# Performance work log

Hardware: AMD Instinct MI355X
Metric: run time of the kernel (lower is better)

## Reference

```python
import jax, jax.numpy as jnp
import numpy as np

B, T, S, D_MODEL = 2, 16, 512, 768
N_HEADS, HEAD_DIM = 12, 64
N_LATENTS = 32


def build_encoder_mask(modality_ids, n_latents):
    # encoder mode: latent queries attend everything; non-latent queries attend same-modality only
    S = modality_ids.shape[0]
    is_q_lat = (jnp.arange(S) < n_latents)[:, None]            # (S,1)
    same_mod = modality_ids[:, None] == modality_ids[None, :]  # (S,S)
    return jnp.where(is_q_lat, True, same_mod)                 # (S,S) bool


def setup_inputs() -> dict:
    key = jax.random.key(0)
    ks = jax.random.split(key, 9)
    x = jax.random.normal(ks[0], (B, T, S, D_MODEL), jnp.float32)
    w_scale = 1.0 / np.sqrt(D_MODEL)
    # flax MultiHeadDotProductAttention param layout: qkv kernels (D, H, head_dim), out kernel (H, head_dim, D)
    Wq = jax.random.normal(ks[1], (D_MODEL, N_HEADS, HEAD_DIM), jnp.float32) * w_scale
    Wk = jax.random.normal(ks[2], (D_MODEL, N_HEADS, HEAD_DIM), jnp.float32) * w_scale
    Wv = jax.random.normal(ks[3], (D_MODEL, N_HEADS, HEAD_DIM), jnp.float32) * w_scale
    Wo = jax.random.normal(ks[4], (N_HEADS, HEAD_DIM, D_MODEL), jnp.float32) * w_scale
    bq = jnp.zeros((N_HEADS, HEAD_DIM), jnp.float32)
    bk = jnp.zeros((N_HEADS, HEAD_DIM), jnp.float32)
    bv = jnp.zeros((N_HEADS, HEAD_DIM), jnp.float32)
    bo = jnp.zeros((D_MODEL,), jnp.float32)
    # 32 latent tokens (id -1), then 240 tokens of modality 0 and 240 of modality 1
    modality_ids = jnp.concatenate([
        jnp.full((N_LATENTS,), -1, jnp.int32),
        jnp.zeros((240,), jnp.int32),
        jnp.ones((240,), jnp.int32),
    ])
    return dict(x=x, Wq=Wq, bq=bq, Wk=Wk, bk=bk, Wv=Wv, bv=bv, Wo=Wo, bo=bo,
                modality_ids=modality_ids, n_latents=N_LATENTS)


def reference(x, Wq, bq, Wk, bk, Wv, bv, Wo, bo, modality_ids, n_latents):
    B, T, S, D = x.shape
    H, hd = Wq.shape[1], Wq.shape[2]
    xf = x.reshape(B * T, S, D)                                   # (BT,S,D)
    q = (jnp.einsum('bsd,dhk->bshk', xf, Wq) + bq) / jnp.sqrt(jnp.asarray(hd, x.dtype))
    k = jnp.einsum('bsd,dhk->bshk', xf, Wk) + bk
    v = jnp.einsum('bsd,dhk->bshk', xf, Wv) + bv
    scores = jnp.einsum('bqhd,bkhd->bhqk', q, k)                  # (BT,H,S,S)
    mask = build_encoder_mask(modality_ids, n_latents)            # (S,S)
    neg = jnp.finfo(x.dtype).min
    scores = jnp.where(mask[None, None], scores, neg)
    attn = jax.nn.softmax(scores, axis=-1)
    ctx = jnp.einsum('bhqk,bkhd->bqhd', attn, v)                  # (BT,S,H,hd)
    y = jnp.einsum('bqhd,hdo->bqo', ctx, Wo) + bo                 # (BT,S,D)
    return y.reshape(B, T, S, D)
```

## Files before the change

### kernel.cpp

```cpp
#include <hip/hip_runtime.h>
#include <hip/hip_bf16.h>
#include <stdint.h>

#define BT_N  32
#define SEQL  512
#define DM    768
#define NHEAD 12
#define HDIM  64
#define MTOT  (BT_N * SEQL)

typedef __bf16 bf16x8 __attribute__((ext_vector_type(8)));
typedef float  f32x4  __attribute__((ext_vector_type(4)));

__device__ __forceinline__ float b2f(uint16_t u)  { return __uint_as_float(((uint32_t)u) << 16); }
__device__ __forceinline__ uint16_t f2b(float f) {
    uint32_t u = __float_as_uint(f);
    return (uint16_t)((u + 0x7fffu + ((u >> 16) & 1u)) >> 16);
}
__device__ __forceinline__ void split_bf16(float x, uint16_t& hi, uint16_t& lo) {
    hi = f2b(x);
    lo = f2b(x - b2f(hi));
}

__global__ __launch_bounds__(256) void split_x_kernel(
    const float* __restrict__ X, uint16_t* __restrict__ Xh, uint16_t* __restrict__ Xl)
{
    size_t i = ((size_t)blockIdx.x * 256 + threadIdx.x) * 4;
    float4 v = *(const float4*)(X + i);
    float xx[4] = {v.x, v.y, v.z, v.w};
    ushort4 h, l;
    uint16_t hh, ll;
    split_bf16(xx[0], hh, ll); h.x = hh; l.x = ll;
    split_bf16(xx[1], hh, ll); h.y = hh; l.y = ll;
    split_bf16(xx[2], hh, ll); h.z = hh; l.z = ll;
    split_bf16(xx[3], hh, ll); h.w = hh; l.w = ll;
    *(ushort4*)(Xh + i) = h;
    *(ushort4*)(Xl + i) = l;
}

__global__ __launch_bounds__(256) void wprep_kernel(
    const float* __restrict__ Wq, const float* __restrict__ Wk,
    const float* __restrict__ Wv, const float* __restrict__ Wo,
    uint16_t* __restrict__ WqTh, uint16_t* __restrict__ WqTl,
    uint16_t* __restrict__ WkTh, uint16_t* __restrict__ WkTl,
    uint16_t* __restrict__ WvT,  uint16_t* __restrict__ WoT)
{
    __shared__ float tile[32][33];
    const int z = blockIdx.z;
    const float* W; uint16_t* Th; uint16_t* Tl;
    if (z == 0)      { W = Wq; Th = WqTh; Tl = WqTl; }
    else if (z == 1) { W = Wk; Th = WkTh; Tl = WkTl; }
    else if (z == 2) { W = Wv; Th = WvT;  Tl = nullptr; }
    else             { W = Wo; Th = WoT;  Tl = nullptr; }

    const int k0 = blockIdx.x * 32, n0 = blockIdx.y * 32;
    const int tid = threadIdx.x;
    {
        int r = tid >> 3, c = (tid & 7) * 4;
        *(float4*)&tile[r][c] = *(const float4*)(W + (size_t)(k0 + r) * DM + n0 + c);
    }
    __syncthreads();
    {
        int nl = tid >> 3, kk = (tid & 7) * 4;
        ushort4 h, l;
        uint16_t hh, ll;
        float v0 = tile[kk + 0][nl], v1 = tile[kk + 1][nl];
        float v2 = tile[kk + 2][nl], v3 = tile[kk + 3][nl];
        split_bf16(v0, hh, ll); h.x = hh; l.x = ll;
        split_bf16(v1, hh, ll); h.y = hh; l.y = ll;
        split_bf16(v2, hh, ll); h.z = hh; l.z = ll;
        split_bf16(v3, hh, ll); h.w = hh; l.w = ll;
        size_t o = (size_t)(n0 + nl) * DM + k0 + kk;
        *(ushort4*)(Th + o) = h;
        if (Tl) *(ushort4*)(Tl + o) = l;
    }
}

__global__ __launch_bounds__(256) void qkv_gemm_v3(
    const uint16_t* __restrict__ Xh, const uint16_t* __restrict__ Xl,
    const uint16_t* __restrict__ WqTh, const uint16_t* __restrict__ WqTl,
    const uint16_t* __restrict__ WkTh, const uint16_t* __restrict__ WkTl,
    const uint16_t* __restrict__ WvT,
    const float* __restrict__ bq, const float* __restrict__ bk, const float* __restrict__ bv,
    uint16_t* __restrict__ Qh, uint16_t* __restrict__ Ql,
    uint16_t* __restrict__ Kh, uint16_t* __restrict__ Kl,
    uint16_t* __restrict__ Vt)
{
    __shared__ uint16_t AhS[128][72], AlS[128][72];
    __shared__ uint16_t BhS[64][72],  BlS[64][72];

    const int m0 = blockIdx.x * 128;
    const int n0 = blockIdx.y * 64;
    const int z  = blockIdx.z;

    const uint16_t* Bh_g; const uint16_t* Bl_g = nullptr; const float* bias;
    if (z == 0)      { Bh_g = WqTh; Bl_g = WqTl; bias = bq; }
    else if (z == 1) { Bh_g = WkTh; Bl_g = WkTl; bias = bk; }
    else             { Bh_g = WvT;               bias = bv; }

    const int tid  = threadIdx.x;
    const int lane = tid & 63, wave = tid >> 6;
    const int quad = lane >> 4, l16 = lane & 15;
    const int wq = wave * 32;

    f32x4 acc[2][4];
    #pragma unroll
    for (int t = 0; t < 2; t++)
        #pragma unroll
        for (int nt = 0; nt < 4; nt++) acc[t][nt] = (f32x4){0.f,0.f,0.f,0.f};

    const int sr = tid >> 3, sc = (tid & 7) * 8;

    for (int k0 = 0; k0 < DM; k0 += 64) {
        __syncthreads();
        #pragma unroll
        for (int i = 0; i < 4; i++) {
            int r = i * 32 + sr;
            *(uint4*)&AhS[r][sc] = *(const uint4*)(Xh + (size_t)(m0 + r) * DM + k0 + sc);
        }
        #pragma unroll
        for (int i = 0; i < 2; i++) {
            int r = i * 32 + sr;
            *(uint4*)&BhS[r][sc] = *(const uint4*)(Bh_g + (size_t)(n0 + r) * DM + k0 + sc);
        }
        if (z < 2) {
            #pragma unroll
            for (int i = 0; i < 4; i++) {
                int r = i * 32 + sr;
                *(uint4*)&AlS[r][sc] = *(const uint4*)(Xl + (size_t)(m0 + r) * DM + k0 + sc);
            }
            #pragma unroll
            for (int i = 0; i < 2; i++) {
                int r = i * 32 + sr;
                *(uint4*)&BlS[r][sc] = *(const uint4*)(Bl_g + (size_t)(n0 + r) * DM + k0 + sc);
            }
        }
        __syncthreads();
        #pragma unroll
        for (int ksub = 0; ksub < 2; ksub++) {
            bf16x8 ah[2], bh[4];
            ah[0] = *(const bf16x8*)&AhS[wq + l16][ksub * 32 + quad * 8];
            ah[1] = *(const bf16x8*)&AhS[wq + 16 + l16][ksub * 32 + quad * 8];
            #pragma unroll
            for (int nt = 0; nt < 4; nt++)
                bh[nt] = *(const bf16x8*)&BhS[nt * 16 + l16][ksub * 32 + quad * 8];
            if (z < 2) {
                bf16x8 al[2], bl[4];
                al[0] = *(const bf16x8*)&AlS[wq + l16][ksub * 32 + quad * 8];
                al[1] = *(const bf16x8*)&AlS[wq + 16 + l16][ksub * 32 + quad * 8];
                #pragma unroll
                for (int nt = 0; nt < 4; nt++)
                    bl[nt] = *(const bf16x8*)&BlS[nt * 16 + l16][ksub * 32 + quad * 8];
                #pragma unroll
                for (int t = 0; t < 2; t++)
                    #pragma unroll
                    for (int nt = 0; nt < 4; nt++) {
                        acc[t][nt] = __builtin_amdgcn_mfma_f32_16x16x32_bf16(al[t], bh[nt], acc[t][nt], 0, 0, 0);
                        acc[t][nt] = __builtin_amdgcn_mfma_f32_16x16x32_bf16(ah[t], bl[nt], acc[t][nt], 0, 0, 0);
                        acc[t][nt] = __builtin_amdgcn_mfma_f32_16x16x32_bf16(ah[t], bh[nt], acc[t][nt], 0, 0, 0);
                    }
            } else {
                #pragma unroll
                for (int t = 0; t < 2; t++)
                    #pragma unroll
                    for (int nt = 0; nt < 4; nt++)
                        acc[t][nt] = __builtin_amdgcn_mfma_f32_16x16x32_bf16(ah[t], bh[nt], acc[t][nt], 0, 0, 0);
            }
        }
    }

    const float scale = (z == 0) ? 0.125f : 1.0f;
    uint16_t* OutH = (z == 0) ? Qh : Kh;
    uint16_t* OutL = (z == 0) ? Ql : Kl;
    #pragma unroll
    for (int t = 0; t < 2; t++) {
        #pragma unroll
        for (int nt = 0; nt < 4; nt++) {
            int n = n0 + nt * 16 + l16;
            float bsv = bias[n];
            int hh = n >> 6, d = n & 63;
            int mbase = m0 + wq + t * 16 + quad * 4;
            if (z == 2) {
                int bt = mbase >> 9, sb = mbase & 511;
                ushort4 pk;
                pk.x = f2b(acc[t][nt][0] + bsv);
                pk.y = f2b(acc[t][nt][1] + bsv);
                pk.z = f2b(acc[t][nt][2] + bsv);
                pk.w = f2b(acc[t][nt][3] + bsv);
                *(ushort4*)&Vt[(((size_t)bt * NHEAD + hh) * HDIM + d) * SEQL + sb] = pk;
            } else {
                #pragma unroll
                for (int r = 0; r < 4; r++) {
                    int m = mbase + r;
                    float val = (acc[t][nt][r] + bsv) * scale;
                    uint16_t vh, vl; split_bf16(val, vh, vl);
                    int bt = m >> 9, s = m & 511;
                    size_t idx = (((size_t)bt * NHEAD + hh) * SEQL + s) * HDIM + d;
                    OutH[idx] = vh; OutL[idx] = vl;
                }
            }
        }
    }
}

__global__ __launch_bounds__(256) void out_proj_v2(
    const uint16_t* __restrict__ A, const uint16_t* __restrict__ WoT,
    const float* __restrict__ bias, float* __restrict__ Y)
{
    __shared__ uint16_t As[128][72];
    __shared__ uint16_t Bs[64][72];

    const int m0 = blockIdx.x * 128;
    const int n0 = blockIdx.y * 64;
    const int tid  = threadIdx.x;
    const int lane = tid & 63, wave = tid >> 6;
    const int quad = lane >> 4, l16 = lane & 15;
    const int wq = wave * 32;

    f32x4 acc[2][4];
    #pragma unroll
    for (int t = 0; t < 2; t++)
        #pragma unroll
        for (int nt = 0; nt < 4; nt++) acc[t][nt] = (f32x4){0.f,0.f,0.f,0.f};

    const int sr = tid >> 3, sc = (tid & 7) * 8;

    for (int k0 = 0; k0 < DM; k0 += 64) {
        __syncthreads();
        #pragma unroll
        for (int i = 0; i < 4; i++) {
            int r = i * 32 + sr;
            *(uint4*)&As[r][sc] = *(const uint4*)(A + (size_t)(m0 + r) * DM + k0 + sc);
        }
        #pragma unroll
        for (int i = 0; i < 2; i++) {
            int r = i * 32 + sr;
            *(uint4*)&Bs[r][sc] = *(const uint4*)(WoT + (size_t)(n0 + r) * DM + k0 + sc);
        }
        __syncthreads();
        #pragma unroll
        for (int ksub = 0; ksub < 2; ksub++) {
            bf16x8 a0 = *(const bf16x8*)&As[wq + l16][ksub * 32 + quad * 8];
            bf16x8 a1 = *(const bf16x8*)&As[wq + 16 + l16][ksub * 32 + quad * 8];
            bf16x8 bf[4];
            #pragma unroll
            for (int nt = 0; nt < 4; nt++)
                bf[nt] = *(const bf16x8*)&Bs[nt * 16 + l16][ksub * 32 + quad * 8];
            #pragma unroll
            for (int nt = 0; nt < 4; nt++) {
                acc[0][nt] = __builtin_amdgcn_mfma_f32_16x16x32_bf16(a0, bf[nt], acc[0][nt], 0, 0, 0);
                acc[1][nt] = __builtin_amdgcn_mfma_f32_16x16x32_bf16(a1, bf[nt], acc[1][nt], 0, 0, 0);
            }
        }
    }

    #pragma unroll
    for (int t = 0; t < 2; t++) {
        #pragma unroll
        for (int nt = 0; nt < 4; nt++) {
            int n = n0 + nt * 16 + l16;
            float bsv = bias[n];
            #pragma unroll
            for (int r = 0; r < 4; r++) {
                int m = m0 + wq + t * 16 + quad * 4 + r;
                Y[(size_t)m * DM + n] = acc[t][nt][r] + bsv;
            }
        }
    }
}

#define QTILE 128

__global__ __launch_bounds__(256) void attn_mfma_kernel(
    const uint16_t* __restrict__ Qhg, const uint16_t* __restrict__ Qlg,
    const uint16_t* __restrict__ Khg, const uint16_t* __restrict__ Klg,
    const uint16_t* __restrict__ Vtg, const int* __restrict__ modality,
    const int* __restrict__ nlat_p, uint16_t* __restrict__ ctx)
{
    __shared__ uint16_t KhS[64][72];
    __shared__ uint16_t KlS[64][72];
    __shared__ uint16_t Vs[64][72];
    __shared__ uint16_t Ps[QTILE][72];
    __shared__ int modk_s[64];

    const int bh = blockIdx.x;
    const int bt = bh / NHEAD, h = bh % NHEAD;
    const int q0 = blockIdx.y * QTILE;
    const int tid = threadIdx.x, lane = tid & 63, wave = tid >> 6;
    const int quad = lane >> 4, l16 = lane & 15;
    const int wq = wave * 32;

    const size_t hb = (size_t)bh * SEQL * HDIM;
    const int nlat = nlat_p[0];

    bf16x8 qh[2][2], ql[2][2];
    #pragma unroll
    for (int t = 0; t < 2; t++)
        #pragma unroll
        for (int ks = 0; ks < 2; ks++) {
            size_t o = hb + (size_t)(q0 + wq + t*16 + l16) * HDIM + ks*32 + quad*8;
            qh[t][ks] = *(const bf16x8*)(Qhg + o);
            ql[t][ks] = *(const bf16x8*)(Qlg + o);
        }

    int  mq[2][4]; bool lat_[2][4];
    #pragma unroll
    for (int t = 0; t < 2; t++)
        #pragma unroll
        for (int r = 0; r < 4; r++) {
            int row = q0 + wq + t*16 + quad*4 + r;
            mq[t][r]   = modality[row];
            lat_[t][r] = row < nlat;
        }

    float mrow[2][4], lrow[2][4];
    #pragma unroll
    for (int t = 0; t < 2; t++)
        #pragma unroll
        for (int r = 0; r < 4; r++) { mrow[t][r] = -3e38f; lrow[t][r] = 0.f; }
    f32x4 O[2][4];
    #pragma unroll
    for (int t = 0; t < 2; t++)
        #pragma unroll
        for (int dt = 0; dt < 4; dt++) O[t][dt] = (f32x4){0.f,0.f,0.f,0.f};

    for (int s0 = 0; s0 < SEQL; s0 += 64) {
        __syncthreads();
        {
            int rr = tid >> 2, c0 = (tid & 3) * 16;
            const uint16_t* kp = Khg + hb + (size_t)(s0 + rr) * HDIM + c0;
            const uint16_t* lp = Klg + hb + (size_t)(s0 + rr) * HDIM + c0;
            const uint16_t* vp = Vtg + hb + (size_t)rr * SEQL + s0 + c0;
            *(uint4*)&KhS[rr][c0]     = *(const uint4*)kp;
            *(uint4*)&KhS[rr][c0 + 8] = *((const uint4*)kp + 1);
            *(uint4*)&KlS[rr][c0]     = *(const uint4*)lp;
            *(uint4*)&KlS[rr][c0 + 8] = *((const uint4*)lp + 1);
            *(uint4*)&Vs[rr][c0]      = *(const uint4*)vp;
            *(uint4*)&Vs[rr][c0 + 8]  = *((const uint4*)vp + 1);
        }
        if (tid < 64) modk_s[tid] = modality[s0 + tid];
        __syncthreads();

        f32x4 S[2][4];
        #pragma unroll
        for (int t = 0; t < 2; t++)
            #pragma unroll
            for (int n = 0; n < 4; n++) S[t][n] = (f32x4){0.f,0.f,0.f,0.f};
        #pragma unroll
        for (int n = 0; n < 4; n++) {
            #pragma unroll
            for (int ks = 0; ks < 2; ks++) {
                bf16x8 kh = *(const bf16x8*)&KhS[n*16 + l16][ks*32 + quad*8];
                bf16x8 kl = *(const bf16x8*)&KlS[n*16 + l16][ks*32 + quad*8];
                #pragma unroll
                for (int t = 0; t < 2; t++) {
                    S[t][n] = __builtin_amdgcn_mfma_f32_16x16x32_bf16(ql[t][ks], kh, S[t][n], 0, 0, 0);
                    S[t][n] = __builtin_amdgcn_mfma_f32_16x16x32_bf16(qh[t][ks], kl, S[t][n], 0, 0, 0);
                    S[t][n] = __builtin_amdgcn_mfma_f32_16x16x32_bf16(qh[t][ks], kh, S[t][n], 0, 0, 0);
                }
            }
        }

        int mk[4];
        #pragma unroll
        for (int n = 0; n < 4; n++) mk[n] = modk_s[n*16 + l16];
        #pragma unroll
        for (int t = 0; t < 2; t++)
            #pragma unroll
            for (int n = 0; n < 4; n++)
                #pragma unroll
                for (int r = 0; r < 4; r++)
                    if (!(lat_[t][r] || (mq[t][r] == mk[n]))) S[t][n][r] = -3e38f;

        #pragma unroll
        for (int t = 0; t < 2; t++) {
            #pragma unroll
            for (int r = 0; r < 4; r++) {
                float mc = fmaxf(fmaxf(S[t][0][r], S[t][1][r]),
                                 fmaxf(S[t][2][r], S[t][3][r]));
                #pragma unroll
                for (int off = 1; off <= 8; off <<= 1)
                    mc = fmaxf(mc, __shfl_xor(mc, off, 64));
                float mo = mrow[t][r];
                float mn = fmaxf(mo, mc);
                float al = __expf(mo - mn);
                float g  = (mn <= -1e37f) ? 0.f : 1.f;
                float sum = 0.f;
                #pragma unroll
                for (int n = 0; n < 4; n++) {
                    float p = __expf(S[t][n][r] - mn) * g;
                    Ps[wq + t*16 + quad*4 + r][n*16 + l16] = f2b(p);
                    sum += p;
                }
                #pragma unroll
                for (int off = 1; off <= 8; off <<= 1)
                    sum += __shfl_xor(sum, off, 64);
                lrow[t][r] = lrow[t][r] * al + sum;
                mrow[t][r] = mn;
                #pragma unroll
                for (int dt = 0; dt < 4; dt++) O[t][dt][r] *= al;
            }
        }

        #pragma unroll
        for (int ks = 0; ks < 2; ks++) {
            bf16x8 pa[2];
            #pragma unroll
            for (int t = 0; t < 2; t++)
                pa[t] = *(const bf16x8*)&Ps[wq + t*16 + l16][ks*32 + quad*8];
            #pragma unroll
            for (int dt = 0; dt < 4; dt++) {
                bf16x8 vb = *(const bf16x8*)&Vs[dt*16 + l16][ks*32 + quad*8];
                #pragma unroll
                for (int t = 0; t < 2; t++)
                    O[t][dt] = __builtin_amdgcn_mfma_f32_16x16x32_bf16(pa[t], vb, O[t][dt], 0, 0, 0);
            }
        }
    }

    #pragma unroll
    for (int t = 0; t < 2; t++) {
        float inv[4];
        #pragma unroll
        for (int r = 0; r < 4; r++) inv[r] = 1.0f / fmaxf(lrow[t][r], 1e-30f);
        #pragma unroll
        for (int dt = 0; dt < 4; dt++) {
            #pragma unroll
            for (int r = 0; r < 4; r++) {
                int row = q0 + wq + t*16 + quad*4 + r;
                ctx[(size_t)(bt * SEQL + row) * DM + h*HDIM + dt*16 + l16] =
                    f2b(O[t][dt][r] * inv[r]);
            }
        }
    }
}

extern "C" void kernel_launch(void* const* d_in, const int* in_sizes, int n_in,
                              void* d_out, int out_size, void* d_ws, size_t ws_size,
                              hipStream_t stream) {
    const float* X  = (const float*)d_in[0];
    const float* Wq = (const float*)d_in[1];
    const float* bq = (const float*)d_in[2];
    const float* Wk = (const float*)d_in[3];
    const float* bk = (const float*)d_in[4];
    const float* Wv = (const float*)d_in[5];
    const float* bv = (const float*)d_in[6];
    const float* Wo = (const float*)d_in[7];
    const float* bo = (const float*)d_in[8];
    const int* modality = (const int*)d_in[9];
    const int* nlat     = (const int*)d_in[10];

    const size_t per = (size_t)MTOT * DM;
    const size_t wsz = (size_t)DM * DM;
    uint16_t* p = (uint16_t*)d_ws;
    uint16_t* Xh   = p; p += per;
    uint16_t* Xl   = p; p += per;
    uint16_t* WqTh = p; p += wsz;
    uint16_t* WqTl = p; p += wsz;
    uint16_t* WkTh = p; p += wsz;
    uint16_t* WkTl = p; p += wsz;
    uint16_t* WvT  = p; p += wsz;
    uint16_t* WoT  = p; p += wsz;
    uint16_t* Qh   = p; p += per;
    uint16_t* Ql   = p; p += per;
    uint16_t* Kh   = p; p += per;
    uint16_t* Kl   = p; p += per;
    uint16_t* Vt   = p; p += per;
    uint16_t* c_ws = Xh;

    split_x_kernel<<<dim3(per / 1024), 256, 0, stream>>>(X, Xh, Xl);
    wprep_kernel<<<dim3(DM / 32, DM / 32, 4), 256, 0, stream>>>(
        Wq, Wk, Wv, Wo, WqTh, WqTl, WkTh, WkTl, WvT, WoT);
    qkv_gemm_v3<<<dim3(MTOT / 128, DM / 64, 3), 256, 0, stream>>>(
        Xh, Xl, WqTh, WqTl, WkTh, WkTl, WvT, bq, bk, bv, Qh, Ql, Kh, Kl, Vt);
    attn_mfma_kernel<<<dim3(BT_N * NHEAD, SEQL / QTILE), 256, 0, stream>>>(
        Qh, Ql, Kh, Kl, Vt, modality, nlat, c_ws);
    out_proj_v2<<<dim3(MTOT / 128, DM / 64), 256, 0, stream>>>(
        c_ws, WoT, bo, (float*)d_out);
}
```

Measured before the change: 475.3 us.

## Rewrite projection GEMMs with 128x128 tiles, double-buffered direct-to-LDS loads and swizzle

The QKV and output projection GEMMs are rebuilt around 128x128 block tiles with a 2x2 wave layout. Global tiles are loaded straight into LDS with global_load_lds into two ping-pong buffers, so the next tile's loads overlap the current tile's MFMAs. An XOR swizzle on the LDS layout avoids bank conflicts. The V projection, which needs only the hi part, moves into its own kernel so the split-precision Q/K path carries no per-iteration branch. The larger tiles raise register pressure, and the launch bound of 2 blocks per SM plus the fixed iteration counts tie the kernels to these exact dimensions.

```diff
diff --git a/kernel.cpp b/kernel.cpp
--- a/kernel.cpp
+++ b/kernel.cpp
@@ -1,5 +1,4 @@
 #include <hip/hip_runtime.h>
-#include <hip/hip_bf16.h>
 #include <stdint.h>
 
 #define BT_N  32
@@ -20,6 +19,13 @@
 __device__ __forceinline__ void split_bf16(float x, uint16_t& hi, uint16_t& lo) {
     hi = f2b(x);
     lo = f2b(x - b2f(hi));
+}
+
+__device__ __forceinline__ void gload16(const void* g, void* l) {
+    __builtin_amdgcn_global_load_lds(
+        (const __attribute__((address_space(1))) void*)g,
+        (__attribute__((address_space(3))) void*)l,
+        16, 0, 0);
 }
 
 __global__ __launch_bounds__(256) void split_x_kernel(
@@ -76,195 +82,318 @@
     }
 }
 
-__global__ __launch_bounds__(256) void qkv_gemm_v3(
+__global__ __launch_bounds__(256, 2) void qk_gemm_split(
     const uint16_t* __restrict__ Xh, const uint16_t* __restrict__ Xl,
     const uint16_t* __restrict__ WqTh, const uint16_t* __restrict__ WqTl,
     const uint16_t* __restrict__ WkTh, const uint16_t* __restrict__ WkTl,
-    const uint16_t* __restrict__ WvT,
-    const float* __restrict__ bq, const float* __restrict__ bk, const float* __restrict__ bv,
+    const float* __restrict__ bq, const float* __restrict__ bk,
     uint16_t* __restrict__ Qh, uint16_t* __restrict__ Ql,
-    uint16_t* __restrict__ Kh, uint16_t* __restrict__ Kl,
-    uint16_t* __restrict__ Vt)
+    uint16_t* __restrict__ Kh, uint16_t* __restrict__ Kl)
 {
-    __shared__ uint16_t AhS[128][72], AlS[128][72];
-    __shared__ uint16_t BhS[64][72],  BlS[64][72];
+    __shared__ uint16_t lds[2][16384];
 
     const int m0 = blockIdx.x * 128;
-    const int n0 = blockIdx.y * 64;
+    const int n0 = blockIdx.y * 128;
     const int z  = blockIdx.z;
 
-    const uint16_t* Bh_g; const uint16_t* Bl_g = nullptr; const float* bias;
-    if (z == 0)      { Bh_g = WqTh; Bl_g = WqTl; bias = bq; }
-    else if (z == 1) { Bh_g = WkTh; Bl_g = WkTl; bias = bk; }
-    else             { Bh_g = WvT;               bias = bv; }
+    const uint16_t* Bh_g = z ? WkTh : WqTh;
+    const uint16_t* Bl_g = z ? WkTl : WqTl;
+    const float* bias    = z ? bk : bq;
+    uint16_t* OutH       = z ? Kh : Qh;
+    uint16_t* OutL       = z ? Kl : Ql;
+    const float scale    = z ? 1.0f : 0.125f;
 
     const int tid  = threadIdx.x;
     const int lane = tid & 63, wave = tid >> 6;
     const int quad = lane >> 4, l16 = lane & 15;
-    const int wq = wave * 32;
-
-    f32x4 acc[2][4];
-    #pragma unroll
-    for (int t = 0; t < 2; t++)
-        #pragma unroll
-        for (int nt = 0; nt < 4; nt++) acc[t][nt] = (f32x4){0.f,0.f,0.f,0.f};
-
-    const int sr = tid >> 3, sc = (tid & 7) * 8;
-
-    for (int k0 = 0; k0 < DM; k0 += 64) {
+    const int wm = (wave >> 1) * 64, wn = (wave & 1) * 64;
+
+    const uint16_t* src[8];
+    #pragma unroll
+    for (int i = 0; i < 8; i++) {
+        int d    = (i * 256 + tid) * 16;
+        int row  = (d >> 7) & 127;
+        int colb = d & 127;
+        int scol = colb ^ ((row & 7) << 4);
+        int kofs = (scol & 63) >> 1;
+        const uint16_t* g;
+        if (d < 16384) g = (scol < 64 ? Xh : Xl)     + (size_t)(m0 + row) * DM + kofs;
+        else           g = (scol < 64 ? Bh_g : Bl_g) + (size_t)(n0 + row) * DM + kofs;
+        src[i] = g;
+    }
+
+    int offA[4], offB[4];
+    #pragma unroll
+    for (int i = 0; i < 4; i++) {
+        int r  = wm + i * 16 + l16;
+        offA[i] = r * 64 + (((quad * 16) ^ ((r & 7) << 4)) >> 1);
+        int rb = wn + i * 16 + l16;
+        offB[i] = 8192 + rb * 64 + (((quad * 16) ^ ((rb & 7) << 4)) >> 1);
+    }
+
+    f32x4 acc[4][4];
+    #pragma unroll
+    for (int i = 0; i < 4; i++)
+        #pragma unroll
+        for (int j = 0; j < 4; j++) acc[i][j] = (f32x4){0.f,0.f,0.f,0.f};
+
+    auto stage = [&](int buf) {
+        #pragma unroll
+        for (int i = 0; i < 8; i++) {
+            gload16(src[i], &lds[buf][(i * 256 + wave * 64) * 8]);
+            src[i] += 32;
+        }
+    };
+    auto computeTile = [&](int buf) {
+        const uint16_t* base = &lds[buf][0];
+        bf16x8 ah[4], al[4], bh[4], bl[4];
+        #pragma unroll
+        for (int i = 0; i < 4; i++) {
+            ah[i] = *(const bf16x8*)(base + offA[i]);
+            al[i] = *(const bf16x8*)(base + (offA[i] ^ 32));
+            bh[i] = *(const bf16x8*)(base + offB[i]);
+            bl[i] = *(const bf16x8*)(base + (offB[i] ^ 32));
+        }
+        #pragma unroll
+        for (int mi = 0; mi < 4; mi++)
+            #pragma unroll
+            for (int ni = 0; ni < 4; ni++) {
+                acc[mi][ni] = __builtin_amdgcn_mfma_f32_16x16x32_bf16(al[mi], bh[ni], acc[mi][ni], 0, 0, 0);
+                acc[mi][ni] = __builtin_amdgcn_mfma_f32_16x16x32_bf16(ah[mi], bl[ni], acc[mi][ni], 0, 0, 0);
+                acc[mi][ni] = __builtin_amdgcn_mfma_f32_16x16x32_bf16(ah[mi], bh[ni], acc[mi][ni], 0, 0, 0);
+            }
+    };
+
+    stage(0);
+    asm volatile("s_waitcnt vmcnt(0)" ::: "memory");
+    __syncthreads();
+
+    int cur = 0;
+    for (int t = 0; t < 23; t++) {
+        stage(cur ^ 1);
+        computeTile(cur);
+        asm volatile("s_waitcnt vmcnt(0)" ::: "memory");
         __syncthreads();
+        cur ^= 1;
+    }
+    computeTile(cur);
+
+    #pragma unroll
+    for (int i = 0; i < 4; i++) {
+        #pragma unroll
+        for (int j = 0; j < 4; j++) {
+            int n = n0 + wn + j * 16 + l16;
+            float bsv = bias[n];
+            int hh = n >> 6, dd = n & 63;
+            int mb = m0 + wm + i * 16 + quad * 4;
+            #pragma unroll
+            for (int r = 0; r < 4; r++) {
+                int m = mb + r;
+                float val = (acc[i][j][r] + bsv) * scale;
+                uint16_t vh, vl; split_bf16(val, vh, vl);
+                int bt = m >> 9, s = m & 511;
+                size_t idx = (((size_t)bt * NHEAD + hh) * SEQL + s) * HDIM + dd;
+                OutH[idx] = vh; OutL[idx] = vl;
+            }
+        }
+    }
+}
+
+__global__ __launch_bounds__(256, 2) void v_gemm_plain(
+    const uint16_t* __restrict__ Xh, const uint16_t* __restrict__ WvT,
+    const float* __restrict__ bv, uint16_t* __restrict__ Vt)
+{
+    __shared__ uint16_t lds[2][16384];
+
+    const int m0 = blockIdx.x * 128;
+    const int n0 = blockIdx.y * 128;
+    const int tid  = threadIdx.x;
+    const int lane = tid & 63, wave = tid >> 6;
+    const int quad = lane >> 4, l16 = lane & 15;
+    const int wm = (wave >> 1) * 64, wn = (wave & 1) * 64;
+
+    const uint16_t* src[8];
+    #pragma unroll
+    for (int i = 0; i < 8; i++) {
+        int d    = (i * 256 + tid) * 16;
+        int row  = (d >> 7) & 127;
+        int colb = d & 127;
+        int scol = colb ^ ((row & 7) << 4);
+        int kofs = scol >> 1;
+        src[i] = (d < 16384 ? Xh + (size_t)(m0 + row) * DM
+                            : WvT + (size_t)(n0 + row) * DM) + kofs;
+    }
+
+    int offA[4], offB[4];
+    #pragma unroll
+    for (int i = 0; i < 4; i++) {
+        int r  = wm + i * 16 + l16;
+        offA[i] = r * 64 + (((quad * 16) ^ ((r & 7) << 4)) >> 1);
+        int rb = wn + i * 16 + l16;
+        offB[i] = 8192 + rb * 64 + (((quad * 16) ^ ((rb & 7) << 4)) >> 1);
+    }
+
+    f32x4 acc[4][4];
+    #pragma unroll
+    for (int i = 0; i < 4; i++)
+        #pragma unroll
+        for (int j = 0; j < 4; j++) acc[i][j] = (f32x4){0.f,0.f,0.f,0.f};
+
+    auto stage = [&](int buf) {
+        #pragma unroll
+        for (int i = 0; i < 8; i++) {
+            gload16(src[i], &lds[buf][(i * 256 + wave * 64) * 8]);
+            src[i] += 64;
+        }
+    };
+    auto computeTile = [&](int buf) {
+        const uint16_t* base = &lds[buf][0];
+        bf16x8 a0[4], a1[4], b0[4], b1[4];
         #pragma unroll
         for (int i = 0; i < 4; i++) {
-            int r = i * 32 + sr;
-            *(uint4*)&AhS[r][sc] = *(const uint4*)(Xh + (size_t)(m0 + r) * DM + k0 + sc);
-        }
-        #pragma unroll
-        for (int i = 0; i < 2; i++) {
-            int r = i * 32 + sr;
-            *(uint4*)&BhS[r][sc] = *(const uint4*)(Bh_g + (size_t)(n0 + r) * DM + k0 + sc);
-        }
-        if (z < 2) {
-            #pragma unroll
-            for (int i = 0; i < 4; i++) {
-                int r = i * 32 + sr;
-                *(uint4*)&AlS[r][sc] = *(const uint4*)(Xl + (size_t)(m0 + r) * DM + k0 + sc);
-            }
-            #pragma unroll
-            for (int i = 0; i < 2; i++) {
-                int r = i * 32 + sr;
-                *(uint4*)&BlS[r][sc] = *(const uint4*)(Bl_g + (size_t)(n0 + r) * DM + k0 + sc);
-            }
-        }
+            a0[i] = *(const bf16x8*)(base + offA[i]);
+            a1[i] = *(const bf16x8*)(base + (offA[i] ^ 32));
+            b0[i] = *(const bf16x8*)(base + offB[i]);
+            b1[i] = *(const bf16x8*)(base + (offB[i] ^ 32));
+        }
+        #pragma unroll
+        for (int mi = 0; mi < 4; mi++)
+            #pragma unroll
+            for (int ni = 0; ni < 4; ni++)
+                acc[mi][ni] = __builtin_amdgcn_mfma_f32_16x16x32_bf16(a0[mi], b0[ni], acc[mi][ni], 0, 0, 0);
+        #pragma unroll
+        for (int mi = 0; mi < 4; mi++)
+            #pragma unroll
+            for (int ni = 0; ni < 4; ni++)
+                acc[mi][ni] = __builtin_amdgcn_mfma_f32_16x16x32_bf16(a1[mi], b1[ni], acc[mi][ni], 0, 0, 0);
+    };
+
+    stage(0);
+    asm volatile("s_waitcnt vmcnt(0)" ::: "memory");
+    __syncthreads();
+
+    int cur = 0;
+    for (int t = 0; t < 11; t++) {
+        stage(cur ^ 1);
+        computeTile(cur);
+        asm volatile("s_waitcnt vmcnt(0)" ::: "memory");
         __syncthreads();
-        #pragma unroll
-        for (int ksub = 0; ksub < 2; ksub++) {
-            bf16x8 ah[2], bh[4];
-            ah[0] = *(const bf16x8*)&AhS[wq + l16][ksub * 32 + quad * 8];
-            ah[1] = *(const bf16x8*)&AhS[wq + 16 + l16][ksub * 32 + quad * 8];
-            #pragma unroll
-            for (int nt = 0; nt < 4; nt++)
-                bh[nt] = *(const bf16x8*)&BhS[nt * 16 + l16][ksub * 32 + quad * 8];
-            if (z < 2) {
-                bf16x8 al[2], bl[4];
-                al[0] = *(const bf16x8*)&AlS[wq + l16][ksub * 32 + quad * 8];
-                al[1] = *(const bf16x8*)&AlS[wq + 16 + l16][ksub * 32 + quad * 8];
-                #pragma unroll
-                for (int nt = 0; nt < 4; nt++)
-                    bl[nt] = *(const bf16x8*)&BlS[nt * 16 + l16][ksub * 32 + quad * 8];
-                #pragma unroll
-                for (int t = 0; t < 2; t++)
-                    #pragma unroll
-                    for (int nt = 0; nt < 4; nt++) {
-                        acc[t][nt] = __builtin_amdgcn_mfma_f32_16x16x32_bf16(al[t], bh[nt], acc[t][nt], 0, 0, 0);
-                        acc[t][nt] = __builtin_amdgcn_mfma_f32_16x16x32_bf16(ah[t], bl[nt], acc[t][nt], 0, 0, 0);
-                        acc[t][nt] = __builtin_amdgcn_mfma_f32_16x16x32_bf16(ah[t], bh[nt], acc[t][nt], 0, 0, 0);
-                    }
-            } else {
-                #pragma unroll
-                for (int t = 0; t < 2; t++)
-                    #pragma unroll
-                    for (int nt = 0; nt < 4; nt++)
-                        acc[t][nt] = __builtin_amdgcn_mfma_f32_16x16x32_bf16(ah[t], bh[nt], acc[t][nt], 0, 0, 0);
-            }
-        }
-    }
-
-    const float scale = (z == 0) ? 0.125f : 1.0f;
-    uint16_t* OutH = (z == 0) ? Qh : Kh;
-    uint16_t* OutL = (z == 0) ? Ql : Kl;
-    #pragma unroll
-    for (int t = 0; t < 2; t++) {
-        #pragma unroll
-        for (int nt = 0; nt < 4; nt++) {
-            int n = n0 + nt * 16 + l16;
-            float bsv = bias[n];
-            int hh = n >> 6, d = n & 63;
-            int mbase = m0 + wq + t * 16 + quad * 4;
-            if (z == 2) {
-                int bt = mbase >> 9, sb = mbase & 511;
-                ushort4 pk;
-                pk.x = f2b(acc[t][nt][0] + bsv);
-                pk.y = f2b(acc[t][nt][1] + bsv);
-                pk.z = f2b(acc[t][nt][2] + bsv);
-                pk.w = f2b(acc[t][nt][3] + bsv);
-                *(ushort4*)&Vt[(((size_t)bt * NHEAD + hh) * HDIM + d) * SEQL + sb] = pk;
-            } else {
-                #pragma unroll
-                for (int r = 0; r < 4; r++) {
-                    int m = mbase + r;
-                    float val = (acc[t][nt][r] + bsv) * scale;
-                    uint16_t vh, vl; split_bf16(val, vh, vl);
-                    int bt = m >> 9, s = m & 511;
-                    size_t idx = (((size_t)bt * NHEAD + hh) * SEQL + s) * HDIM + d;
-                    OutH[idx] = vh; OutL[idx] = vl;
-                }
-            }
-        }
-    }
-}
-
-__global__ __launch_bounds__(256) void out_proj_v2(
+        cur ^= 1;
+    }
+    computeTile(cur);
+
+    #pragma unroll
+    for (int i = 0; i < 4; i++) {
+        #pragma unroll
+        for (int j = 0; j < 4; j++) {
+            int n = n0 + wn + j * 16 + l16;
+            float bsv = bv[n];
+            int hh = n >> 6, dd = n & 63;
+            int mb = m0 + wm + i * 16 + quad * 4;
+            int bt = mb >> 9, sb = mb & 511;
+            ushort4 pk;
+            pk.x = f2b(acc[i][j][0] + bsv);
+            pk.y = f2b(acc[i][j][1] + bsv);
+            pk.z = f2b(acc[i][j][2] + bsv);
+            pk.w = f2b(acc[i][j][3] + bsv);
+            *(ushort4*)&Vt[(((size_t)bt * NHEAD + hh) * HDIM + dd) * SEQL + sb] = pk;
+        }
+    }
+}
+
+__global__ __launch_bounds__(256, 2) void out_proj_v3(
     const uint16_t* __restrict__ A, const uint16_t* __restrict__ WoT,
     const float* __restrict__ bias, float* __restrict__ Y)
 {
-    __shared__ uint16_t As[128][72];
-    __shared__ uint16_t Bs[64][72];
+    __shared__ uint16_t lds[2][16384];
 
     const int m0 = blockIdx.x * 128;
-    const int n0 = blockIdx.y * 64;
+    const int n0 = blockIdx.y * 128;
     const int tid  = threadIdx.x;
     const int lane = tid & 63, wave = tid >> 6;
     const int quad = lane >> 4, l16 = lane & 15;
-    const int wq = wave * 32;
-
-    f32x4 acc[2][4];
-    #pragma unroll
-    for (int t = 0; t < 2; t++)
-        #pragma unroll
-        for (int nt = 0; nt < 4; nt++) acc[t][nt] = (f32x4){0.f,0.f,0.f,0.f};
-
-    const int sr = tid >> 3, sc = (tid & 7) * 8;
-
-    for (int k0 = 0; k0 < DM; k0 += 64) {
+    const int wm = (wave >> 1) * 64, wn = (wave & 1) * 64;
+
+    const uint16_t* src[8];
+    #pragma unroll
+    for (int i = 0; i < 8; i++) {
+        int d    = (i * 256 + tid) * 16;
+        int row  = (d >> 7) & 127;
+        int colb = d & 127;
+        int scol = colb ^ ((row & 7) << 4);
+        int kofs = scol >> 1;
+        src[i] = (d < 16384 ? A + (size_t)(m0 + row) * DM
+                            : WoT + (size_t)(n0 + row) * DM) + kofs;
+    }
+
+    int offA[4], offB[4];
+    #pragma unroll
+    for (int i = 0; i < 4; i++) {
+        int r  = wm + i * 16 + l16;
+        offA[i] = r * 64 + (((quad * 16) ^ ((r & 7) << 4)) >> 1);
+        int rb = wn + i * 16 + l16;
+        offB[i] = 8192 + rb * 64 + (((quad * 16) ^ ((rb & 7) << 4)) >> 1);
+    }
+
+    f32x4 acc[4][4];
+    #pragma unroll
+    for (int i = 0; i < 4; i++)
+        #pragma unroll
+        for (int j = 0; j < 4; j++) acc[i][j] = (f32x4){0.f,0.f,0.f,0.f};
+
+    auto stage = [&](int buf) {
+        #pragma unroll
+        for (int i = 0; i < 8; i++) {
+            gload16(src[i], &lds[buf][(i * 256 + wave * 64) * 8]);
+            src[i] += 64;
+        }
+    };
+    auto computeTile = [&](int buf) {
+        const uint16_t* base = &lds[buf][0];
+        bf16x8 a0[4], a1[4], b0[4], b1[4];
+        #pragma unroll
+        for (int i = 0; i < 4; i++) {
+            a0[i] = *(const bf16x8*)(base + offA[i]);
+            a1[i] = *(const bf16x8*)(base + (offA[i] ^ 32));
+            b0[i] = *(const bf16x8*)(base + offB[i]);
+            b1[i] = *(const bf16x8*)(base + (offB[i] ^ 32));
+        }
+        #pragma unroll
+        for (int mi = 0; mi < 4; mi++)
+            #pragma unroll
+            for (int ni = 0; ni < 4; ni++)
+                acc[mi][ni] = __builtin_amdgcn_mfma_f32_16x16x32_bf16(a0[mi], b0[ni], acc[mi][ni], 0, 0, 0);
+        #pragma unroll
+        for (int mi = 0; mi < 4; mi++)
+            #pragma unroll
+            for (int ni = 0; ni < 4; ni++)
+                acc[mi][ni] = __builtin_amdgcn_mfma_f32_16x16x32_bf16(a1[mi], b1[ni], acc[mi][ni], 0, 0, 0);
+    };
+
+    stage(0);
+    asm volatile("s_waitcnt vmcnt(0)" ::: "memory");
+    __syncthreads();
+
+    int cur = 0;
+    for (int t = 0; t < 11; t++) {
+        stage(cur ^ 1);
+        computeTile(cur);
+        asm volatile("s_waitcnt vmcnt(0)" ::: "memory");
         __syncthreads();
-        #pragma unroll
-        for (int i = 0; i < 4; i++) {
-            int r = i * 32 + sr;
-            *(uint4*)&As[r][sc] = *(const uint4*)(A + (size_t)(m0 + r) * DM + k0 + sc);
-        }
-        #pragma unroll
-        for (int i = 0; i < 2; i++) {
-            int r = i * 32 + sr;
-            *(uint4*)&Bs[r][sc] = *(const uint4*)(WoT + (size_t)(n0 + r) * DM + k0 + sc);
-        }
-        __syncthreads();
-        #pragma unroll
-        for (int ksub = 0; ksub < 2; ksub++) {
-            bf16x8 a0 = *(const bf16x8*)&As[wq + l16][ksub * 32 + quad * 8];
-            bf16x8 a1 = *(const bf16x8*)&As[wq + 16 + l16][ksub * 32 + quad * 8];
-            bf16x8 bf[4];
-            #pragma unroll
-            for (int nt = 0; nt < 4; nt++)
-                bf[nt] = *(const bf16x8*)&Bs[nt * 16 + l16][ksub * 32 + quad * 8];
-            #pragma unroll
-            for (int nt = 0; nt < 4; nt++) {
-                acc[0][nt] = __builtin_amdgcn_mfma_f32_16x16x32_bf16(a0, bf[nt], acc[0][nt], 0, 0, 0);
-                acc[1][nt] = __builtin_amdgcn_mfma_f32_16x16x32_bf16(a1, bf[nt], acc[1][nt], 0, 0, 0);
-            }
-        }
-    }
-
-    #pragma unroll
-    for (int t = 0; t < 2; t++) {
-        #pragma unroll
-        for (int nt = 0; nt < 4; nt++) {
-            int n = n0 + nt * 16 + l16;
+        cur ^= 1;
+    }
+    computeTile(cur);
+
+    #pragma unroll
+    for (int i = 0; i < 4; i++) {
+        #pragma unroll
+        for (int j = 0; j < 4; j++) {
+            int n = n0 + wn + j * 16 + l16;
             float bsv = bias[n];
-            #pragma unroll
-            for (int r = 0; r < 4; r++) {
-                int m = m0 + wq + t * 16 + quad * 4 + r;
-                Y[(size_t)m * DM + n] = acc[t][nt][r] + bsv;
-            }
+            int mb = m0 + wm + i * 16 + quad * 4;
+            #pragma unroll
+            for (int r = 0; r < 4; r++)
+                Y[(size_t)(mb + r) * DM + n] = acc[i][j][r] + bsv;
         }
     }
 }
@@ -471,10 +600,12 @@
     split_x_kernel<<<dim3(per / 1024), 256, 0, stream>>>(X, Xh, Xl);
     wprep_kernel<<<dim3(DM / 32, DM / 32, 4), 256, 0, stream>>>(
         Wq, Wk, Wv, Wo, WqTh, WqTl, WkTh, WkTl, WvT, WoT);
-    qkv_gemm_v3<<<dim3(MTOT / 128, DM / 64, 3), 256, 0, stream>>>(
-        Xh, Xl, WqTh, WqTl, WkTh, WkTl, WvT, bq, bk, bv, Qh, Ql, Kh, Kl, Vt);
+    qk_gemm_split<<<dim3(MTOT / 128, DM / 128, 2), 256, 0, stream>>>(
+        Xh, Xl, WqTh, WqTl, WkTh, WkTl, bq, bk, Qh, Ql, Kh, Kl);
+    v_gemm_plain<<<dim3(MTOT / 128, DM / 128), 256, 0, stream>>>(
+        Xh, WvT, bv, Vt);
     attn_mfma_kernel<<<dim3(BT_N * NHEAD, SEQL / QTILE), 256, 0, stream>>>(
         Qh, Ql, Kh, Kl, Vt, modality, nlat, c_ws);
-    out_proj_v2<<<dim3(MTOT / 128, DM / 64), 256, 0, stream>>>(
+    out_proj_v3<<<dim3(MTOT / 128, DM / 128), 256, 0, stream>>>(
         c_ws, WoT, bo, (float*)d_out);
 }
```

Result: faster. 437.8 us (-7.9%).
